# Kernel tuning notes

Hardware: AMD Instinct MI355X
Metric: run time of the kernel (lower is better)

The kernel has to match this reference:

```python
import jax, jax.numpy as jnp
import numpy as np

D = 512; NH = 8; NL = 6; DFF = 2048
TOK = 1024; APP = 3; V = TOK + APP; PAD = V - 1
B = 256; SENC = 16; LTGT = 62


def setup_inputs() -> dict:
    key = jax.random.key(0)
    ks = jax.random.split(key, 14)
    g = lambda k, shp, s=0.02: jax.random.normal(k, shp, jnp.float32) * s
    return dict(
        encoder_out=jax.random.normal(ks[0], (B, SENC, D), jnp.float32),
        point_out=jax.random.normal(ks[1], (B, D), jnp.float32),
        emb=g(ks[2], (V, D)),
        pos_embed=g(ks[3], (1, LTGT, D)),
        sa_inw=g(ks[4], (NL, 3 * D, D)), sa_inb=jnp.zeros((NL, 3 * D), jnp.float32),
        sa_outw=g(ks[5], (NL, D, D)), sa_outb=jnp.zeros((NL, D), jnp.float32),
        ca_inw=g(ks[6], (NL, 3 * D, D)), ca_inb=jnp.zeros((NL, 3 * D), jnp.float32),
        ca_outw=g(ks[7], (NL, D, D)), ca_outb=jnp.zeros((NL, D), jnp.float32),
        ln1_s=jnp.ones((NL, D), jnp.float32), ln1_b=jnp.zeros((NL, D), jnp.float32),
        ln2_s=jnp.ones((NL, D), jnp.float32), ln2_b=jnp.zeros((NL, D), jnp.float32),
        ln3_s=jnp.ones((NL, D), jnp.float32), ln3_b=jnp.zeros((NL, D), jnp.float32),
        ff1_w=g(ks[8], (NL, DFF, D)), ff1_b=jnp.zeros((NL, DFF), jnp.float32),
        ff2_w=g(ks[9], (NL, D, DFF)), ff2_b=jnp.zeros((NL, D), jnp.float32),
        out_w=g(ks[10], (V, D)), out_b=jnp.zeros((V,), jnp.float32),
        tgt=jax.random.randint(ks[11], (B, LTGT), 0, TOK),
    )


def _ln(x, s, b, eps=1e-5):
    m = x.mean(-1, keepdims=True)
    v = ((x - m) ** 2).mean(-1, keepdims=True)
    return (x - m) / jnp.sqrt(v + eps) * s + b


def _mha(q_in, kv_in, inw, inb, outw, outb, mask):
    # PyTorch MultiheadAttention with packed in_proj [3D, D]
    hd = D // NH
    wq, wk, wv = inw[:D], inw[D:2 * D], inw[2 * D:]
    bq, bk, bv = inb[:D], inb[D:2 * D], inb[2 * D:]
    Bq, Tq = q_in.shape[0], q_in.shape[1]
    Tk = kv_in.shape[1]
    q = (q_in @ wq.T + bq).reshape(Bq, Tq, NH, hd)
    k = (kv_in @ wk.T + bk).reshape(Bq, Tk, NH, hd)
    v = (kv_in @ wv.T + bv).reshape(Bq, Tk, NH, hd)
    s = jnp.einsum('bqhd,bkhd->bhqk', q, k) / np.float32(np.sqrt(hd))
    if mask is not None:
        s = s + mask
    a = jax.nn.softmax(s, axis=-1)
    o = jnp.einsum('bhqk,bkhd->bqhd', a, v).reshape(Bq, Tq, D)
    return o @ outw.T + outb


def reference(encoder_out, point_out, emb, pos_embed,
              sa_inw, sa_inb, sa_outw, sa_outb,
              ca_inw, ca_inb, ca_outw, ca_outb,
              ln1_s, ln1_b, ln2_s, ln2_b, ln3_s, ln3_b,
              ff1_w, ff1_b, ff2_w, ff2_b, out_w, out_b, tgt):
    # scheduled_sampling_ratio == 1.0 => the per-step loop always writes the
    # ground-truth token, so output_sequence == tgt[:, :-1] and the returned
    # tensor equals one full causal decoder pass over tgt[:, :-1].
    tokens = tgt[:, :-1]                      # [B, L], L = 61
    L = tokens.shape[1]
    neg = jnp.float32(-jnp.inf)
    causal = jnp.where(jnp.triu(jnp.ones((L, L), bool), 1), neg, 0.0)
    padm = jnp.where(tokens == PAD, neg, 0.0)[:, None, None, :]  # [B,1,1,L]
    mask = causal[None, None] + padm          # [B,1,L,L]
    mem = encoder_out[:, :1, :]               # memory length 1 (encoder_out[:, [0]])
    x = emb[tokens] + point_out[:, None, :] + pos_embed[0, :L]
    for i in range(NL):
        x = _ln(x + _mha(x, x, sa_inw[i], sa_inb[i], sa_outw[i], sa_outb[i], mask), ln1_s[i], ln1_b[i])
        x = _ln(x + _mha(x, mem, ca_inw[i], ca_inb[i], ca_outw[i], ca_outb[i], None), ln2_s[i], ln2_b[i])
        h = jax.nn.relu(x @ ff1_w[i].T + ff1_b[i]) @ ff2_w[i].T + ff2_b[i]
        x = _ln(x + h, ln3_s[i], ln3_b[i])
    return x @ out_w.T + out_b               # [B, L, V]
```

## Files before the change

kernel.cpp:

```cpp
#include <hip/hip_runtime.h>
#include <stdint.h>
#include <stddef.h>

typedef unsigned short u16;
typedef float f4 __attribute__((ext_vector_type(4)));
typedef float f32x4 __attribute__((ext_vector_type(4)));
typedef short bf16x8 __attribute__((ext_vector_type(8)));
typedef u16 u16x4 __attribute__((ext_vector_type(4)));
typedef int i4v __attribute__((ext_vector_type(4)));

#define PAD_TOK 1026
#define LQ 61
#define NBATCH 256
#define MTOT (NBATCH * LQ)

__device__ __forceinline__ u16 f2b(float f) {
  uint32_t x = __float_as_uint(f);
  x += 0x7fff + ((x >> 16) & 1);
  return (u16)(x >> 16);
}
__device__ __forceinline__ float b2f(u16 u) {
  return __uint_as_float(((uint32_t)u) << 16);
}

#define GLDS(gptr, lptr) __builtin_amdgcn_global_load_lds( \
    (const __attribute__((address_space(1))) void*)(gptr), \
    (__attribute__((address_space(3))) void*)(lptr), 16, 0, 0)

__device__ __forceinline__ bf16x8 ldfrag(const u16* buf, int row, int ksl, int kg) {
  const int chunk = (ksl * 4 + kg) ^ (row & 7);
  return *(const bf16x8*)&buf[row * 64 + chunk * 8];
}

template<int BM>
__global__ __launch_bounds__(256) void gemm_bt(
    const u16* __restrict__ A, const u16* __restrict__ W,
    const float* __restrict__ bias,
    float* __restrict__ Cf, u16* __restrict__ Cb,
    int M, int N, int K, int Nreal, int ldc, int relu,
    long aZ, long wZ, long bZ, long cZ)
{
  constexpr int MI = BM / 32;
  const int z = blockIdx.z;
  A += z * aZ; W += z * wZ; bias += z * bZ;
  if (Cf) Cf += z * cZ;
  if (Cb) Cb += z * cZ;

  __shared__ u16 As[BM * 64];
  __shared__ u16 Bs[128 * 64];

  const int gx = gridDim.x;
  const int nwg = gx * gridDim.y;
  const int orig = blockIdx.y * gx + blockIdx.x;
  const int q8 = nwg >> 3, r8 = nwg & 7;
  const int xcd = orig & 7, off = orig >> 3;
  const int nid = (xcd < r8 ? xcd * (q8 + 1) : r8 * (q8 + 1) + (xcd - r8) * q8) + off;
  const int bx = nid % gx, by = nid / gx;

  const int tid = threadIdx.x;
  const int wid = tid >> 6, lane = tid & 63;
  const int wr = wid >> 1, wc = wid & 1;
  const long m0 = (long)by * BM;
  const long n0 = (long)bx * 128;

  const int lr = lane >> 3;
  const int lc = lane & 7;
  const int scol = ((lc ^ lr) << 3);

  f32x4 acc[MI][4];
#pragma unroll
  for (int i = 0; i < MI; ++i)
#pragma unroll
    for (int j = 0; j < 4; ++j) acc[i][j] = (f32x4){0.f, 0.f, 0.f, 0.f};

  const u16* Abase = A + m0 * K;
  const u16* Wbase = W + n0 * K;
  const int r = lane & 15, kg = lane >> 4;

  for (int kt = 0; kt < K; kt += 64) {
#pragma unroll
    for (int c = 0; c < BM / 32; ++c) {
      const int row = wid * (BM / 4) + c * 8;
      GLDS(Abase + (long)(row + lr) * K + kt + scol, &As[row * 64]);
    }
#pragma unroll
    for (int c = 0; c < 4; ++c) {
      const int row = wid * 32 + c * 8;
      GLDS(Wbase + (long)(row + lr) * K + kt + scol, &Bs[row * 64]);
    }
    __syncthreads();

#pragma unroll
    for (int ks = 0; ks < 2; ++ks) {
      bf16x8 a[MI], b[4];
#pragma unroll
      for (int mi = 0; mi < MI; ++mi)
        a[mi] = ldfrag(As, wr * (BM / 2) + mi * 16 + r, ks, kg);
#pragma unroll
      for (int ni = 0; ni < 4; ++ni)
        b[ni] = ldfrag(Bs, wc * 64 + ni * 16 + r, ks, kg);
#pragma unroll
      for (int mi = 0; mi < MI; ++mi)
#pragma unroll
        for (int ni = 0; ni < 4; ++ni)
          acc[mi][ni] = __builtin_amdgcn_mfma_f32_16x16x32_bf16(a[mi], b[ni], acc[mi][ni], 0, 0, 0);
    }
    __syncthreads();
  }

  const int cr4 = (lane >> 4) * 4;
  const int cc = lane & 15;

  if (Cb) {
#pragma unroll
    for (int ni = 0; ni < 4; ++ni) {
      const int coll = wc * 64 + ni * 16 + cc;
      const float bv = bias[(int)n0 + coll];
#pragma unroll
      for (int mi = 0; mi < MI; ++mi) {
#pragma unroll
        for (int j = 0; j < 4; ++j) {
          const int rowl = wr * (BM / 2) + mi * 16 + cr4 + j;
          float v = acc[mi][ni][j] + bv;
          if (relu) v = fmaxf(v, 0.f);
          const int sw = (rowl & 7) << 3;
          u16* half = (coll & 64) ? Bs : As;
          half[rowl * 64 + ((coll & 63) ^ sw)] = f2b(v);
        }
      }
    }
    __syncthreads();
    constexpr int PT = BM / 16;
#pragma unroll
    for (int i = 0; i < PT; ++i) {
      const int t = i * 256 + tid;
      const int row = t >> 4, ch = t & 15;
      const int n = (int)n0 + ch * 8;
      if (n < Nreal) {
        const int phys = (ch & 7) ^ (row & 7);
        const u16* half = (ch < 8) ? As : Bs;
        bf16x8 vv = *(const bf16x8*)&half[row * 64 + phys * 8];
        *(bf16x8*)&Cb[(m0 + row) * (long)N + n] = vv;
      }
    }
  } else {
#pragma unroll
    for (int ni = 0; ni < 4; ++ni) {
      const int n = (int)n0 + wc * 64 + ni * 16 + cc;
      if (n >= Nreal) continue;
      const float bv = bias[n];
#pragma unroll
      for (int mi = 0; mi < MI; ++mi) {
#pragma unroll
        for (int j = 0; j < 4; ++j) {
          const long m = m0 + wr * (BM / 2) + mi * 16 + cr4 + j;
          float v = acc[mi][ni][j] + bv;
          if (relu) v = fmaxf(v, 0.f);
          Cf[m * ldc + n] = v;
        }
      }
    }
  }
}

template<bool CA2>
__global__ __launch_bounds__(512) void gemmln_k(
    const u16* __restrict__ A, const u16* __restrict__ W,
    const float* __restrict__ bias,
    const u16* __restrict__ cavb,
    const float* __restrict__ s1w, const float* __restrict__ b1w,
    const float* __restrict__ s2w, const float* __restrict__ b2w,
    u16* __restrict__ XB, int K)
{
  __shared__ u16 LDSBUF[2][36864];
  __shared__ float LSTAT[64][8];
  __shared__ u16 LCAV[1536];
  u16* const EP = &LDSBUF[0][0];

  const int nwg = gridDim.x;
  const int orig = blockIdx.x;
  const int q8 = nwg >> 3, r8 = nwg & 7;
  const int xcd = orig & 7, off = orig >> 3;
  const int by = (xcd < r8 ? xcd * (q8 + 1) : r8 * (q8 + 1) + (xcd - r8) * q8) + off;

  const int tid = threadIdx.x;
  const int wid = tid >> 6, lane = tid & 63;
  const int wm = wid >> 2, wn = wid & 3;
  const long m0 = (long)by * 64;

  const int lr = lane >> 3, lc = lane & 7;
  const int scol = ((lc ^ lr) << 3);
  const int r = lane & 15, kg = lane >> 4;

  f32x4 acc[2][8];
#pragma unroll
  for (int i = 0; i < 2; ++i)
#pragma unroll
    for (int j = 0; j < 8; ++j) acc[i][j] = (f32x4){0.f, 0.f, 0.f, 0.f};

  const u16* Abase = A + m0 * K;

#define STAGE(buf, kt) do {                                              \
    const int arow_ = wid * 8;                                           \
    GLDS(Abase + (long)(arow_ + lr) * K + (kt) + scol,                   \
         &(buf)[32768 + arow_ * 64]);                                    \
    _Pragma("unroll")                                                    \
    for (int c_ = 0; c_ < 8; ++c_) {                                     \
      const int row_ = wid * 64 + c_ * 8;                                \
      GLDS(W + (long)(row_ + lr) * K + (kt) + scol, &(buf)[row_ * 64]);  \
    }                                                                    \
  } while (0)

  const int nt = K >> 6;
  STAGE(LDSBUF[0], 0);
  asm volatile("s_waitcnt vmcnt(0)" ::: "memory");
  __builtin_amdgcn_sched_barrier(0);
  __builtin_amdgcn_s_barrier();

  for (int t = 0; t < nt; ++t) {
    u16* const bufc = &LDSBUF[t & 1][0];
    if (t + 1 < nt) STAGE(LDSBUF[(t + 1) & 1], (t + 1) << 6);
#pragma unroll
    for (int ks = 0; ks < 2; ++ks) {
      bf16x8 a0 = ldfrag(bufc + 32768, wm * 32 + r, ks, kg);
      bf16x8 a1 = ldfrag(bufc + 32768, wm * 32 + 16 + r, ks, kg);
      __builtin_amdgcn_s_setprio(1);
#pragma unroll
      for (int ni = 0; ni < 8; ++ni) {
        bf16x8 b = ldfrag(bufc, wn * 128 + ni * 16 + r, ks, kg);
        acc[0][ni] = __builtin_amdgcn_mfma_f32_16x16x32_bf16(a0, b, acc[0][ni], 0, 0, 0);
        acc[1][ni] = __builtin_amdgcn_mfma_f32_16x16x32_bf16(a1, b, acc[1][ni], 0, 0, 0);
      }
      __builtin_amdgcn_s_setprio(0);
    }
    asm volatile("s_waitcnt vmcnt(0)" ::: "memory");
    __builtin_amdgcn_sched_barrier(0);
    __builtin_amdgcn_s_barrier();
  }
#undef STAGE

  const int b0 = (int)(m0 / LQ);
  const int bsplit1 = (b0 + 1) * LQ;
  const int bsplit2 = (b0 + 2) * LQ;

#pragma unroll
  for (int i = 0; i < 8; ++i) {
    const int t = i * 512 + tid;
    const int row = t >> 6, ch = t & 63;
    *(bf16x8*)&EP[row * 516 + ch * 8] =
        *(const bf16x8*)&XB[(m0 + row) * 512 + ch * 8];
  }
  if constexpr (CA2) {
    for (int t = tid; t < 1536; t += 512) {
      const int bb = t >> 9, c = t & 511;
      int bi = b0 + bb;
      if (bi > NBATCH - 1) bi = NBATCH - 1;
      LCAV[bb * 512 + c] = cavb[(long)bi * 512 + c];
    }
  }
  __syncthreads();

  float bcol[8];
#pragma unroll
  for (int ni = 0; ni < 8; ++ni) bcol[ni] = bias[wn * 128 + ni * 16 + r];
#pragma unroll
  for (int mi = 0; mi < 2; ++mi)
#pragma unroll
    for (int ni = 0; ni < 8; ++ni) {
      const int col = wn * 128 + ni * 16 + r;
#pragma unroll
      for (int j = 0; j < 4; ++j) {
        const int row = wm * 32 + mi * 16 + kg * 4 + j;
        acc[mi][ni][j] += bcol[ni] + b2f(EP[row * 516 + col]);
      }
    }

#pragma unroll
  for (int mi = 0; mi < 2; ++mi)
#pragma unroll
    for (int j = 0; j < 4; ++j) {
      float s1 = 0.f, s2 = 0.f;
#pragma unroll
      for (int ni = 0; ni < 8; ++ni) {
        const float v = acc[mi][ni][j];
        s1 += v; s2 += v * v;
      }
#pragma unroll
      for (int o = 1; o < 16; o <<= 1) {
        s1 += __shfl_xor(s1, o);
        s2 += __shfl_xor(s2, o);
      }
      if (r == 0) {
        const int row = wm * 32 + mi * 16 + kg * 4 + j;
        LSTAT[row][wn] = s1;
        LSTAT[row][4 + wn] = s2;
      }
    }
  __syncthreads();

  float sc[8], bc[8];
#pragma unroll
  for (int ni = 0; ni < 8; ++ni) {
    const int col = wn * 128 + ni * 16 + r;
    sc[ni] = s1w[col]; bc[ni] = b1w[col];
  }
#pragma unroll
  for (int mi = 0; mi < 2; ++mi)
#pragma unroll
    for (int j = 0; j < 4; ++j) {
      const int row = wm * 32 + mi * 16 + kg * 4 + j;
      const float S1 = LSTAT[row][0] + LSTAT[row][1] + LSTAT[row][2] + LSTAT[row][3];
      const float S2 = LSTAT[row][4] + LSTAT[row][5] + LSTAT[row][6] + LSTAT[row][7];
      const float mean = S1 * (1.f / 512.f);
      const float var = S2 * (1.f / 512.f) - mean * mean;
      const float rstd = rsqrtf(var + 1e-5f);
#pragma unroll
      for (int ni = 0; ni < 8; ++ni)
        acc[mi][ni][j] = (acc[mi][ni][j] - mean) * rstd * sc[ni] + bc[ni];
    }

  if constexpr (CA2) {
#pragma unroll
    for (int mi = 0; mi < 2; ++mi)
#pragma unroll
      for (int j = 0; j < 4; ++j) {
        const int row = wm * 32 + mi * 16 + kg * 4 + j;
        const int gr = (int)m0 + row;
        const int sel = (gr >= bsplit2) ? 2 : ((gr >= bsplit1) ? 1 : 0);
#pragma unroll
        for (int ni = 0; ni < 8; ++ni) {
          const int col = wn * 128 + ni * 16 + r;
          acc[mi][ni][j] += b2f(LCAV[sel * 512 + col]);
        }
      }
    __syncthreads();
#pragma unroll
    for (int mi = 0; mi < 2; ++mi)
#pragma unroll
      for (int j = 0; j < 4; ++j) {
        float s1 = 0.f, s2 = 0.f;
#pragma unroll
        for (int ni = 0; ni < 8; ++ni) {
          const float v = acc[mi][ni][j];
          s1 += v; s2 += v * v;
        }
#pragma unroll
        for (int o = 1; o < 16; o <<= 1) {
          s1 += __shfl_xor(s1, o);
          s2 += __shfl_xor(s2, o);
        }
        if (r == 0) {
          const int row = wm * 32 + mi * 16 + kg * 4 + j;
          LSTAT[row][wn] = s1;
          LSTAT[row][4 + wn] = s2;
        }
      }
    __syncthreads();
#pragma unroll
    for (int ni = 0; ni < 8; ++ni) {
      const int col = wn * 128 + ni * 16 + r;
      sc[ni] = s2w[col]; bc[ni] = b2w[col];
    }
#pragma unroll
    for (int mi = 0; mi < 2; ++mi)
#pragma unroll
      for (int j = 0; j < 4; ++j) {
        const int row = wm * 32 + mi * 16 + kg * 4 + j;
        const float S1 = LSTAT[row][0] + LSTAT[row][1] + LSTAT[row][2] + LSTAT[row][3];
        const float S2 = LSTAT[row][4] + LSTAT[row][5] + LSTAT[row][6] + LSTAT[row][7];
        const float mean = S1 * (1.f / 512.f);
        const float var = S2 * (1.f / 512.f) - mean * mean;
        const float rstd = rsqrtf(var + 1e-5f);
#pragma unroll
        for (int ni = 0; ni < 8; ++ni)
          acc[mi][ni][j] = (acc[mi][ni][j] - mean) * rstd * sc[ni] + bc[ni];
      }
  }

#pragma unroll
  for (int mi = 0; mi < 2; ++mi)
#pragma unroll
    for (int ni = 0; ni < 8; ++ni) {
      const int col = wn * 128 + ni * 16 + r;
#pragma unroll
      for (int j = 0; j < 4; ++j) {
        const int row = wm * 32 + mi * 16 + kg * 4 + j;
        EP[row * 516 + col] = f2b(acc[mi][ni][j]);
      }
    }
  __syncthreads();
#pragma unroll
  for (int i = 0; i < 8; ++i) {
    const int t = i * 512 + tid;
    const int row = t >> 6, ch = t & 63;
    *(bf16x8*)&XB[(m0 + row) * 512 + ch * 8] =
        *(const bf16x8*)&EP[row * 516 + ch * 8];
  }
}

__global__ __launch_bounds__(256) void attn_k(const u16* __restrict__ qkv,
                                              const int* __restrict__ tgt,
                                              u16* __restrict__ outp)
{
  __shared__ u16 Qs[64 * 72];
  __shared__ u16 Ks[64 * 72];
  __shared__ u16 Vt[64 * 72];
  __shared__ float S[64 * 65];
  __shared__ int stok[64];

  const int bid = blockIdx.x;
  const int b = bid >> 3, h = bid & 7;
  const int tid = threadIdx.x;
  const int tr = tid >> 2, seg = tid & 3;

  if (tid < 64) stok[tid] = (tid < 61) ? tgt[b * 62 + tid] : -1;

  const long rowbase = ((long)(b * LQ + tr)) * 1536 + h * 64;
  if (tr < LQ) {
    const i4v* qsrc = (const i4v*)(qkv + rowbase + seg * 16);
    i4v q0 = qsrc[0], q1 = qsrc[1];
    *(i4v*)&Qs[tr * 72 + seg * 16] = q0;
    *(i4v*)&Qs[tr * 72 + seg * 16 + 8] = q1;
    const i4v* ksrc = (const i4v*)(qkv + rowbase + 512 + seg * 16);
    i4v k0 = ksrc[0], k1 = ksrc[1];
    *(i4v*)&Ks[tr * 72 + seg * 16] = k0;
    *(i4v*)&Ks[tr * 72 + seg * 16 + 8] = k1;
    const u16* vsrc = qkv + rowbase + 1024 + seg * 16;
#pragma unroll
    for (int i = 0; i < 16; ++i) Vt[(seg * 16 + i) * 72 + tr] = vsrc[i];
  } else {
    i4v zz = {0, 0, 0, 0};
    *(i4v*)&Qs[tr * 72 + seg * 16] = zz;
    *(i4v*)&Qs[tr * 72 + seg * 16 + 8] = zz;
    *(i4v*)&Ks[tr * 72 + seg * 16] = zz;
    *(i4v*)&Ks[tr * 72 + seg * 16 + 8] = zz;
#pragma unroll
    for (int i = 0; i < 16; ++i) Vt[(seg * 16 + i) * 72 + tr] = 0;
  }
  __syncthreads();

  const int lane = tid & 63, w = tid >> 6;
  const int r = lane & 15, kg = lane >> 4;

  {
    f32x4 s[4];
#pragma unroll
    for (int ni = 0; ni < 4; ++ni) s[ni] = (f32x4){0.f, 0.f, 0.f, 0.f};
    bf16x8 a0 = *(const bf16x8*)&Qs[(w * 16 + r) * 72 + kg * 8];
    bf16x8 a1 = *(const bf16x8*)&Qs[(w * 16 + r) * 72 + 32 + kg * 8];
#pragma unroll
    for (int ni = 0; ni < 4; ++ni) {
      bf16x8 b0 = *(const bf16x8*)&Ks[(ni * 16 + r) * 72 + kg * 8];
      bf16x8 b1 = *(const bf16x8*)&Ks[(ni * 16 + r) * 72 + 32 + kg * 8];
      s[ni] = __builtin_amdgcn_mfma_f32_16x16x32_bf16(a0, b0, s[ni], 0, 0, 0);
      s[ni] = __builtin_amdgcn_mfma_f32_16x16x32_bf16(a1, b1, s[ni], 0, 0, 0);
    }
#pragma unroll
    for (int ni = 0; ni < 4; ++ni)
#pragma unroll
      for (int j = 0; j < 4; ++j)
        S[(w * 16 + kg * 4 + j) * 65 + ni * 16 + r] = s[ni][j];
  }
  __syncthreads();

  {
    const int row = tid >> 2, g = tid & 3;
    float vals[16];
    float mx = -3e38f;
#pragma unroll
    for (int i = 0; i < 16; ++i) {
      const int k = g * 16 + i;
      float v = S[row * 65 + k] * 0.125f;
      const bool ok = (k <= row) && (k < LQ) && (stok[k] != PAD_TOK);
      v = ok ? v : -1e30f;
      vals[i] = v;
      mx = fmaxf(mx, v);
    }
    mx = fmaxf(mx, __shfl_xor(mx, 1));
    mx = fmaxf(mx, __shfl_xor(mx, 2));
    float sum = 0.f;
#pragma unroll
    for (int i = 0; i < 16; ++i) { float e = __expf(vals[i] - mx); vals[i] = e; sum += e; }
    sum += __shfl_xor(sum, 1);
    sum += __shfl_xor(sum, 2);
    const float inv = 1.f / sum;
#pragma unroll
    for (int i = 0; i < 16; ++i) Qs[row * 72 + g * 16 + i] = f2b(vals[i] * inv);
  }
  __syncthreads();

  {
    f32x4 o[4];
#pragma unroll
    for (int ni = 0; ni < 4; ++ni) o[ni] = (f32x4){0.f, 0.f, 0.f, 0.f};
    bf16x8 a0 = *(const bf16x8*)&Qs[(w * 16 + r) * 72 + kg * 8];
    bf16x8 a1 = *(const bf16x8*)&Qs[(w * 16 + r) * 72 + 32 + kg * 8];
#pragma unroll
    for (int ni = 0; ni < 4; ++ni) {
      bf16x8 b0 = *(const bf16x8*)&Vt[(ni * 16 + r) * 72 + kg * 8];
      bf16x8 b1 = *(const bf16x8*)&Vt[(ni * 16 + r) * 72 + 32 + kg * 8];
      o[ni] = __builtin_amdgcn_mfma_f32_16x16x32_bf16(a0, b0, o[ni], 0, 0, 0);
      o[ni] = __builtin_amdgcn_mfma_f32_16x16x32_bf16(a1, b1, o[ni], 0, 0, 0);
    }
#pragma unroll
    for (int ni = 0; ni < 4; ++ni)
#pragma unroll
      for (int j = 0; j < 4; ++j) {
        const int qrow = w * 16 + kg * 4 + j;
        const int col = ni * 16 + r;
        Ks[qrow * 64 + (col ^ ((qrow & 7) << 3))] = f2b(o[ni][j]);
      }
  }
  __syncthreads();

  {
    const int row = tid >> 2, sub = tid & 3;
    if (row < LQ) {
      const long obase = ((long)(b * LQ + row)) * 512 + h * 64;
#pragma unroll
      for (int i = 0; i < 2; ++i) {
        const int ch = i * 4 + sub;
        const int phys = ch ^ (row & 7);
        bf16x8 vv = *(const bf16x8*)&Ks[row * 64 + phys * 8];
        *(bf16x8*)&outp[obase + ch * 8] = vv;
      }
    }
  }
}

__global__ __launch_bounds__(256) void embed_k(const float* __restrict__ emb,
                                               const float* __restrict__ pout,
                                               const float* __restrict__ pos,
                                               const int* __restrict__ tgt,
                                               u16* __restrict__ XB)
{
  const int m = blockIdx.x * 4 + (threadIdx.x >> 6);
  const int lane = threadIdx.x & 63;
  const int b = m / LQ, t = m % LQ;
  const int tok = tgt[b * 62 + t];
  const int d0 = lane * 8;
  const f4* e = (const f4*)(emb + (long)tok * 512 + d0);
  const f4* p = (const f4*)(pout + (long)b * 512 + d0);
  const f4* q = (const f4*)(pos + (long)t * 512 + d0);
  f4 v0 = e[0] + p[0] + q[0];
  f4 v1 = e[1] + p[1] + q[1];
  u16x4* xb = (u16x4*)(XB + (long)m * 512 + d0);
  xb[0] = (u16x4){f2b(v0[0]), f2b(v0[1]), f2b(v0[2]), f2b(v0[3])};
  xb[1] = (u16x4){f2b(v1[0]), f2b(v1[1]), f2b(v1[2]), f2b(v1[3])};
}

__global__ void cvtall_k(const float* __restrict__ s0, const float* __restrict__ s1,
                         const float* __restrict__ s2, const float* __restrict__ s3,
                         const float* __restrict__ s4,
                         u16* __restrict__ d0, u16* __restrict__ d1,
                         u16* __restrict__ d2, u16* __restrict__ d3,
                         u16* __restrict__ d4)
{
  const int N0 = 1179648;
  const int N1 = N0 + 393216;
  const int N2 = N1 + 393216;
  const int N3 = N2 + 1572864;
  const int N4 = N3 + 1572864;
  for (int i = blockIdx.x * 256 + threadIdx.x; i < N4; i += gridDim.x * 256) {
    const float* s; u16* d; int k;
    if (i < N0)      { s = s0; d = d0; k = i; }
    else if (i < N1) { s = s1; d = d1; k = i - N0; }
    else if (i < N2) { s = s2; d = d2; k = i - N1; }
    else if (i < N3) { s = s3; d = d3; k = i - N2; }
    else             { s = s4; d = d4; k = i - N3; }
    f4 v = ((const f4*)s)[k];
    ((u16x4*)d)[k] = (u16x4){f2b(v[0]), f2b(v[1]), f2b(v[2]), f2b(v[3])};
  }
}

__global__ void cvt_ca_v_k(const float* __restrict__ ca_inw, u16* __restrict__ dst) {
  const int i = blockIdx.x * 256 + threadIdx.x;
  if (i >= 393216) return;
  const int l = i >> 16, rem = i & 65535;
  f4 v = ((const f4*)ca_inw)[l * 196608 + 131072 + rem];
  ((u16x4*)dst)[i] = (u16x4){f2b(v[0]), f2b(v[1]), f2b(v[2]), f2b(v[3])};
}

__global__ void cvt_outw_k(const float* __restrict__ out_w, u16* __restrict__ dst) {
  const int i = blockIdx.x * 256 + threadIdx.x;
  if (i >= 147456) return;
  const int row = (i * 4) >> 9;
  u16x4 o = {0, 0, 0, 0};
  if (row < 1027) {
    f4 v = ((const f4*)out_w)[i];
    o = (u16x4){f2b(v[0]), f2b(v[1]), f2b(v[2]), f2b(v[3])};
  }
  ((u16x4*)dst)[i] = o;
}

__global__ void cvt_outb_k(const float* __restrict__ out_b, float* __restrict__ dst) {
  const int i = blockIdx.x * 256 + threadIdx.x;
  if (i >= 1152) return;
  dst[i] = (i < 1027) ? out_b[i] : 0.f;
}

__global__ void cvt_memb_k(const float* __restrict__ enc, u16* __restrict__ dst) {
  const int i = blockIdx.x * 256 + threadIdx.x;
  if (i >= 32768) return;
  const int b = (i * 4) >> 9, d = (i * 4) & 511;
  f4 v = ((const f4*)enc)[(b * 8192 + d) >> 2];
  ((u16x4*)dst)[i] = (u16x4){f2b(v[0]), f2b(v[1]), f2b(v[2]), f2b(v[3])};
}

static constexpr size_t XB_OFF    = 0;
static constexpr size_t BIG_OFF   = 15990784;
static constexpr size_t ATT_OFF   = 79953920;
static constexpr size_t WSA_OFF   = 95944704;
static constexpr size_t WSO_OFF   = 105381888;
static constexpr size_t WCAV_OFF  = 108527616;
static constexpr size_t WCO_OFF   = 111673344;
static constexpr size_t WF1_OFF   = 114819072;
static constexpr size_t WF2_OFF   = 127401984;
static constexpr size_t WOUT_OFF  = 139984896;
static constexpr size_t BOUT_OFF  = 141164544;
static constexpr size_t MEMB_OFF  = 141169152;
static constexpr size_t CATMP_OFF = 141431296;
static constexpr size_t CAVB_OFF  = 143004160;

extern "C" void kernel_launch(void* const* d_in, const int* in_sizes, int n_in,
                              void* d_out, int out_size, void* d_ws, size_t ws_size,
                              hipStream_t stream) {
  (void)in_sizes; (void)n_in; (void)out_size; (void)ws_size;
  const float* encoder_out = (const float*)d_in[0];
  const float* point_out   = (const float*)d_in[1];
  const float* emb         = (const float*)d_in[2];
  const float* pos         = (const float*)d_in[3];
  const float* sa_inw      = (const float*)d_in[4];
  const float* sa_inb      = (const float*)d_in[5];
  const float* sa_outw     = (const float*)d_in[6];
  const float* sa_outb     = (const float*)d_in[7];
  const float* ca_inw      = (const float*)d_in[8];
  const float* ca_inb      = (const float*)d_in[9];
  const float* ca_outw     = (const float*)d_in[10];
  const float* ca_outb     = (const float*)d_in[11];
  const float* ln1_s       = (const float*)d_in[12];
  const float* ln1_b       = (const float*)d_in[13];
  const float* ln2_s       = (const float*)d_in[14];
  const float* ln2_b       = (const float*)d_in[15];
  const float* ln3_s       = (const float*)d_in[16];
  const float* ln3_b       = (const float*)d_in[17];
  const float* ff1_w       = (const float*)d_in[18];
  const float* ff1_b       = (const float*)d_in[19];
  const float* ff2_w       = (const float*)d_in[20];
  const float* ff2_b       = (const float*)d_in[21];
  const float* out_w       = (const float*)d_in[22];
  const float* out_b       = (const float*)d_in[23];
  const int*   tgt         = (const int*)d_in[24];

  char* ws = (char*)d_ws;
  u16*   XB    = (u16*)(ws + XB_OFF);
  u16*   BIG   = (u16*)(ws + BIG_OFF);
  u16*   ATT   = (u16*)(ws + ATT_OFF);
  u16*   WSA   = (u16*)(ws + WSA_OFF);
  u16*   WSO   = (u16*)(ws + WSO_OFF);
  u16*   WCAV  = (u16*)(ws + WCAV_OFF);
  u16*   WCO   = (u16*)(ws + WCO_OFF);
  u16*   WF1   = (u16*)(ws + WF1_OFF);
  u16*   WF2   = (u16*)(ws + WF2_OFF);
  u16*   WOUT  = (u16*)(ws + WOUT_OFF);
  float* BOUT  = (float*)(ws + BOUT_OFF);
  u16*   MEMB  = (u16*)(ws + MEMB_OFF);
  u16*   CATMP = (u16*)(ws + CATMP_OFF);
  u16*   CAVB  = (u16*)(ws + CAVB_OFF);

  cvtall_k<<<dim3(2048), dim3(256), 0, stream>>>(
      sa_inw, sa_outw, ca_outw, ff1_w, ff2_w, WSA, WSO, WCO, WF1, WF2);
  cvt_ca_v_k<<<dim3(1536), dim3(256), 0, stream>>>(ca_inw, WCAV);
  cvt_outw_k<<<dim3(576), dim3(256), 0, stream>>>(out_w, WOUT);
  cvt_outb_k<<<dim3(5), dim3(256), 0, stream>>>(out_b, BOUT);
  cvt_memb_k<<<dim3(128), dim3(256), 0, stream>>>(encoder_out, MEMB);

  embed_k<<<dim3(MTOT / 4), dim3(256), 0, stream>>>(emb, point_out, pos, tgt, XB);

  gemm_bt<64><<<dim3(4, 4, 6), dim3(256), 0, stream>>>(
      MEMB, WCAV, ca_inb + 1024, nullptr, CATMP,
      256, 512, 512, 512, 512, 0,
      0L, 262144L, 1536L, 131072L);
  gemm_bt<64><<<dim3(4, 4, 6), dim3(256), 0, stream>>>(
      CATMP, WCO, ca_outb, nullptr, CAVB,
      256, 512, 512, 512, 512, 0,
      131072L, 262144L, 512L, 131072L);

  for (int l = 0; l < 6; ++l) {
    gemm_bt<128><<<dim3(12, 122, 1), dim3(256), 0, stream>>>(
        XB, WSA + (long)l * 786432, sa_inb + l * 1536, nullptr, BIG,
        MTOT, 1536, 512, 1536, 1536, 0, 0L, 0L, 0L, 0L);
    attn_k<<<dim3(2048), dim3(256), 0, stream>>>(BIG, tgt, ATT);
    gemmln_k<true><<<dim3(244), dim3(512), 0, stream>>>(
        ATT, WSO + (long)l * 262144, sa_outb + l * 512,
        CAVB + (long)l * 131072,
        ln1_s + l * 512, ln1_b + l * 512, ln2_s + l * 512, ln2_b + l * 512,
        XB, 512);
    gemm_bt<128><<<dim3(16, 122, 1), dim3(256), 0, stream>>>(
        XB, WF1 + (long)l * 1048576, ff1_b + l * 2048, nullptr, BIG,
        MTOT, 2048, 512, 2048, 2048, 1, 0L, 0L, 0L, 0L);
    gemmln_k<false><<<dim3(244), dim3(512), 0, stream>>>(
        BIG, WF2 + (long)l * 1048576, ff2_b + l * 512,
        nullptr,
        ln3_s + l * 512, ln3_b + l * 512, nullptr, nullptr,
        XB, 2048);
  }

  gemm_bt<128><<<dim3(9, 122, 1), dim3(256), 0, stream>>>(
      XB, WOUT, BOUT, (float*)d_out, nullptr,
      MTOT, 1152, 512, 1027, 1027, 0, 0L, 0L, 0L, 0L);
}
```

Measured before the change: 1.291 ms.

## Add 128x256 GEMM kernel and split FF2 GEMM from its layernorm

Result: faster. 1.124 ms (-13.0%).

```diff
diff --git a/kernel.cpp b/kernel.cpp
--- a/kernel.cpp
+++ b/kernel.cpp
@@ -30,6 +30,133 @@
 __device__ __forceinline__ bf16x8 ldfrag(const u16* buf, int row, int ksl, int kg) {
   const int chunk = (ksl * 4 + kg) ^ (row & 7);
   return *(const bf16x8*)&buf[row * 64 + chunk * 8];
+}
+
+__global__ __launch_bounds__(512) void gemm_bt2(
+    const u16* __restrict__ A, const u16* __restrict__ W,
+    const float* __restrict__ bias,
+    float* __restrict__ Cf, u16* __restrict__ Cb,
+    int N, int K, int Nreal, int ldc, int relu)
+{
+  __shared__ u16 SH[384 * 64];
+  u16* const As = SH;
+  u16* const Bs = SH + 8192;
+
+  const int gx = gridDim.x;
+  const int nwg = gx * gridDim.y;
+  const int orig = blockIdx.y * gx + blockIdx.x;
+  const int q8 = nwg >> 3, r8 = nwg & 7;
+  const int xcd = orig & 7, off = orig >> 3;
+  const int nid = (xcd < r8 ? xcd * (q8 + 1) : r8 * (q8 + 1) + (xcd - r8) * q8) + off;
+  const int bx = nid % gx, by = nid / gx;
+
+  const int tid = threadIdx.x;
+  const int wid = tid >> 6, lane = tid & 63;
+  const int wm = wid >> 2, wn = wid & 3;
+  const long m0 = (long)by * 128;
+  const long n0 = (long)bx * 256;
+
+  const int lr = lane >> 3;
+  const int lc = lane & 7;
+  const int scol = ((lc ^ lr) << 3);
+
+  f32x4 acc[4][4];
+#pragma unroll
+  for (int i = 0; i < 4; ++i)
+#pragma unroll
+    for (int j = 0; j < 4; ++j) acc[i][j] = (f32x4){0.f, 0.f, 0.f, 0.f};
+
+  const u16* Abase = A + m0 * K;
+  const u16* Wbase = W + n0 * K;
+  const int r = lane & 15, kg = lane >> 4;
+
+  for (int kt = 0; kt < K; kt += 64) {
+#pragma unroll
+    for (int c = 0; c < 2; ++c) {
+      const int row = wid * 16 + c * 8;
+      GLDS(Abase + (long)(row + lr) * K + kt + scol, &As[row * 64]);
+    }
+#pragma unroll
+    for (int c = 0; c < 4; ++c) {
+      const int row = wid * 32 + c * 8;
+      GLDS(Wbase + (long)(row + lr) * K + kt + scol, &Bs[row * 64]);
+    }
+    __syncthreads();
+
+#pragma unroll
+    for (int ks = 0; ks < 2; ++ks) {
+      bf16x8 a[4], b[4];
+#pragma unroll
+      for (int mi = 0; mi < 4; ++mi)
+        a[mi] = ldfrag(As, wm * 64 + mi * 16 + r, ks, kg);
+#pragma unroll
+      for (int ni = 0; ni < 4; ++ni)
+        b[ni] = ldfrag(Bs, wn * 64 + ni * 16 + r, ks, kg);
+#pragma unroll
+      for (int mi = 0; mi < 4; ++mi)
+#pragma unroll
+        for (int ni = 0; ni < 4; ++ni)
+          acc[mi][ni] = __builtin_amdgcn_mfma_f32_16x16x32_bf16(a[mi], b[ni], acc[mi][ni], 0, 0, 0);
+    }
+    __syncthreads();
+  }
+
+  const int cr4 = (lane >> 4) * 4;
+  const int cc = lane & 15;
+
+  if (Cb) {
+#pragma unroll
+    for (int half = 0; half < 2; ++half) {
+      if (wm == half) {
+#pragma unroll
+        for (int ni = 0; ni < 4; ++ni) {
+          const int coll = wn * 64 + ni * 16 + cc;
+          const float bv = bias[(int)n0 + coll];
+#pragma unroll
+          for (int mi = 0; mi < 4; ++mi) {
+#pragma unroll
+            for (int j = 0; j < 4; ++j) {
+              const int rowl = mi * 16 + cr4 + j;
+              float v = acc[mi][ni][j] + bv;
+              if (relu) v = fmaxf(v, 0.f);
+              const int phys = (coll >> 3) ^ (rowl & 31);
+              SH[rowl * 256 + phys * 8 + (coll & 7)] = f2b(v);
+            }
+          }
+        }
+      }
+      __syncthreads();
+#pragma unroll
+      for (int i = 0; i < 4; ++i) {
+        const int t = i * 512 + tid;
+        const int row = t >> 5, ch = t & 31;
+        const int n = (int)n0 + ch * 8;
+        if (n < Nreal) {
+          const int phys = ch ^ (row & 31);
+          *(bf16x8*)&Cb[(m0 + half * 64 + row) * (long)N + n] =
+              *(const bf16x8*)&SH[row * 256 + phys * 8];
+        }
+      }
+      __syncthreads();
+    }
+  } else {
+#pragma unroll
+    for (int ni = 0; ni < 4; ++ni) {
+      const int n = (int)n0 + wn * 64 + ni * 16 + cc;
+      if (n >= Nreal) continue;
+      const float bv = bias[n];
+#pragma unroll
+      for (int mi = 0; mi < 4; ++mi) {
+#pragma unroll
+        for (int j = 0; j < 4; ++j) {
+          const long m = m0 + wm * 64 + mi * 16 + cr4 + j;
+          float v = acc[mi][ni][j] + bv;
+          if (relu) v = fmaxf(v, 0.f);
+          Cf[m * ldc + n] = v;
+        }
+      }
+    }
+  }
 }
 
 template<int BM>
@@ -163,7 +290,6 @@
   }
 }
 
-template<bool CA2>
 __global__ __launch_bounds__(512) void gemmln_k(
     const u16* __restrict__ A, const u16* __restrict__ W,
     const float* __restrict__ bias,
@@ -250,13 +376,11 @@
     *(bf16x8*)&EP[row * 516 + ch * 8] =
         *(const bf16x8*)&XB[(m0 + row) * 512 + ch * 8];
   }
-  if constexpr (CA2) {
-    for (int t = tid; t < 1536; t += 512) {
-      const int bb = t >> 9, c = t & 511;
-      int bi = b0 + bb;
-      if (bi > NBATCH - 1) bi = NBATCH - 1;
-      LCAV[bb * 512 + c] = cavb[(long)bi * 512 + c];
-    }
+  for (int t = tid; t < 1536; t += 512) {
+    const int bb = t >> 9, c = t & 511;
+    int bi = b0 + bb;
+    if (bi > NBATCH - 1) bi = NBATCH - 1;
+    LCAV[bb * 512 + c] = cavb[(long)bi * 512 + c];
   }
   __syncthreads();
 
@@ -319,63 +443,61 @@
         acc[mi][ni][j] = (acc[mi][ni][j] - mean) * rstd * sc[ni] + bc[ni];
     }
 
-  if constexpr (CA2) {
-#pragma unroll
-    for (int mi = 0; mi < 2; ++mi)
-#pragma unroll
-      for (int j = 0; j < 4; ++j) {
+#pragma unroll
+  for (int mi = 0; mi < 2; ++mi)
+#pragma unroll
+    for (int j = 0; j < 4; ++j) {
+      const int row = wm * 32 + mi * 16 + kg * 4 + j;
+      const int gr = (int)m0 + row;
+      const int sel = (gr >= bsplit2) ? 2 : ((gr >= bsplit1) ? 1 : 0);
+#pragma unroll
+      for (int ni = 0; ni < 8; ++ni) {
+        const int col = wn * 128 + ni * 16 + r;
+        acc[mi][ni][j] += b2f(LCAV[sel * 512 + col]);
+      }
+    }
+  __syncthreads();
+#pragma unroll
+  for (int mi = 0; mi < 2; ++mi)
+#pragma unroll
+    for (int j = 0; j < 4; ++j) {
+      float s1 = 0.f, s2 = 0.f;
+#pragma unroll
+      for (int ni = 0; ni < 8; ++ni) {
+        const float v = acc[mi][ni][j];
+        s1 += v; s2 += v * v;
+      }
+#pragma unroll
+      for (int o = 1; o < 16; o <<= 1) {
+        s1 += __shfl_xor(s1, o);
+        s2 += __shfl_xor(s2, o);
+      }
+      if (r == 0) {
         const int row = wm * 32 + mi * 16 + kg * 4 + j;
-        const int gr = (int)m0 + row;
-        const int sel = (gr >= bsplit2) ? 2 : ((gr >= bsplit1) ? 1 : 0);
-#pragma unroll
-        for (int ni = 0; ni < 8; ++ni) {
-          const int col = wn * 128 + ni * 16 + r;
-          acc[mi][ni][j] += b2f(LCAV[sel * 512 + col]);
-        }
-      }
-    __syncthreads();
-#pragma unroll
-    for (int mi = 0; mi < 2; ++mi)
-#pragma unroll
-      for (int j = 0; j < 4; ++j) {
-        float s1 = 0.f, s2 = 0.f;
-#pragma unroll
-        for (int ni = 0; ni < 8; ++ni) {
-          const float v = acc[mi][ni][j];
-          s1 += v; s2 += v * v;
-        }
-#pragma unroll
-        for (int o = 1; o < 16; o <<= 1) {
-          s1 += __shfl_xor(s1, o);
-          s2 += __shfl_xor(s2, o);
-        }
-        if (r == 0) {
-          const int row = wm * 32 + mi * 16 + kg * 4 + j;
-          LSTAT[row][wn] = s1;
-          LSTAT[row][4 + wn] = s2;
-        }
-      }
-    __syncthreads();
-#pragma unroll
-    for (int ni = 0; ni < 8; ++ni) {
-      const int col = wn * 128 + ni * 16 + r;
-      sc[ni] = s2w[col]; bc[ni] = b2w[col];
-    }
-#pragma unroll
-    for (int mi = 0; mi < 2; ++mi)
-#pragma unroll
-      for (int j = 0; j < 4; ++j) {
-        const int row = wm * 32 + mi * 16 + kg * 4 + j;
-        const float S1 = LSTAT[row][0] + LSTAT[row][1] + LSTAT[row][2] + LSTAT[row][3];
-        const float S2 = LSTAT[row][4] + LSTAT[row][5] + LSTAT[row][6] + LSTAT[row][7];
-        const float mean = S1 * (1.f / 512.f);
-        const float var = S2 * (1.f / 512.f) - mean * mean;
-        const float rstd = rsqrtf(var + 1e-5f);
-#pragma unroll
-        for (int ni = 0; ni < 8; ++ni)
-          acc[mi][ni][j] = (acc[mi][ni][j] - mean) * rstd * sc[ni] + bc[ni];
-      }
-  }
+        LSTAT[row][wn] = s1;
+        LSTAT[row][4 + wn] = s2;
+      }
+    }
+  __syncthreads();
+#pragma unroll
+  for (int ni = 0; ni < 8; ++ni) {
+    const int col = wn * 128 + ni * 16 + r;
+    sc[ni] = s2w[col]; bc[ni] = b2w[col];
+  }
+#pragma unroll
+  for (int mi = 0; mi < 2; ++mi)
+#pragma unroll
+    for (int j = 0; j < 4; ++j) {
+      const int row = wm * 32 + mi * 16 + kg * 4 + j;
+      const float S1 = LSTAT[row][0] + LSTAT[row][1] + LSTAT[row][2] + LSTAT[row][3];
+      const float S2 = LSTAT[row][4] + LSTAT[row][5] + LSTAT[row][6] + LSTAT[row][7];
+      const float mean = S1 * (1.f / 512.f);
+      const float var = S2 * (1.f / 512.f) - mean * mean;
+      const float rstd = rsqrtf(var + 1e-5f);
+#pragma unroll
+      for (int ni = 0; ni < 8; ++ni)
+        acc[mi][ni][j] = (acc[mi][ni][j] - mean) * rstd * sc[ni] + bc[ni];
+    }
 
 #pragma unroll
   for (int mi = 0; mi < 2; ++mi)
@@ -526,6 +648,53 @@
       }
     }
   }
+}
+
+__device__ __forceinline__ void ln_row(f4& v0, f4& v1,
+                                       const float* __restrict__ sw,
+                                       const float* __restrict__ bw, int d0) {
+  float s1 = v0[0] + v0[1] + v0[2] + v0[3] + v1[0] + v1[1] + v1[2] + v1[3];
+  float s2 = v0[0]*v0[0] + v0[1]*v0[1] + v0[2]*v0[2] + v0[3]*v0[3]
+           + v1[0]*v1[0] + v1[1]*v1[1] + v1[2]*v1[2] + v1[3]*v1[3];
+#pragma unroll
+  for (int off = 1; off < 64; off <<= 1) {
+    s1 += __shfl_xor(s1, off);
+    s2 += __shfl_xor(s2, off);
+  }
+  const float mean = s1 * (1.f / 512.f);
+  const float var = s2 * (1.f / 512.f) - mean * mean;
+  const float rstd = rsqrtf(var + 1e-5f);
+  const f4* sp = (const f4*)(sw + d0);
+  const f4* bp = (const f4*)(bw + d0);
+  f4 ss0 = sp[0], ss1 = sp[1], bb0 = bp[0], bb1 = bp[1];
+#pragma unroll
+  for (int i = 0; i < 4; ++i) {
+    v0[i] = (v0[i] - mean) * rstd * ss0[i] + bb0[i];
+    v1[i] = (v1[i] - mean) * rstd * ss1[i] + bb1[i];
+  }
+}
+
+__global__ __launch_bounds__(256) void lnf3_k(const u16* __restrict__ p,
+                                              const u16* __restrict__ xr,
+                                              const float* __restrict__ s1,
+                                              const float* __restrict__ b1,
+                                              u16* __restrict__ out)
+{
+  const int m = blockIdx.x * 4 + (threadIdx.x >> 6);
+  const int lane = threadIdx.x & 63;
+  const int d0 = lane * 8;
+  bf16x8 pv = *(const bf16x8*)(p + (long)m * 512 + d0);
+  bf16x8 xv = *(const bf16x8*)(xr + (long)m * 512 + d0);
+  f4 v0, v1;
+#pragma unroll
+  for (int i = 0; i < 4; ++i) {
+    v0[i] = b2f((u16)pv[i]) + b2f((u16)xv[i]);
+    v1[i] = b2f((u16)pv[4 + i]) + b2f((u16)xv[4 + i]);
+  }
+  ln_row(v0, v1, s1, b1, d0);
+  u16x4* ob = (u16x4*)(out + (long)m * 512 + d0);
+  ob[0] = (u16x4){f2b(v0[0]), f2b(v0[1]), f2b(v0[2]), f2b(v0[3])};
+  ob[1] = (u16x4){f2b(v1[0]), f2b(v1[1]), f2b(v1[2]), f2b(v1[3])};
 }
 
 __global__ __launch_bounds__(256) void embed_k(const float* __restrict__ emb,
@@ -583,7 +752,7 @@
 
 __global__ void cvt_outw_k(const float* __restrict__ out_w, u16* __restrict__ dst) {
   const int i = blockIdx.x * 256 + threadIdx.x;
-  if (i >= 147456) return;
+  if (i >= 163840) return;
   const int row = (i * 4) >> 9;
   u16x4 o = {0, 0, 0, 0};
   if (row < 1027) {
@@ -595,7 +764,7 @@
 
 __global__ void cvt_outb_k(const float* __restrict__ out_b, float* __restrict__ dst) {
   const int i = blockIdx.x * 256 + threadIdx.x;
-  if (i >= 1152) return;
+  if (i >= 1280) return;
   dst[i] = (i < 1027) ? out_b[i] : 0.f;
 }
 
@@ -608,19 +777,20 @@
 }
 
 static constexpr size_t XB_OFF    = 0;
-static constexpr size_t BIG_OFF   = 15990784;
-static constexpr size_t ATT_OFF   = 79953920;
-static constexpr size_t WSA_OFF   = 95944704;
-static constexpr size_t WSO_OFF   = 105381888;
-static constexpr size_t WCAV_OFF  = 108527616;
-static constexpr size_t WCO_OFF   = 111673344;
-static constexpr size_t WF1_OFF   = 114819072;
-static constexpr size_t WF2_OFF   = 127401984;
-static constexpr size_t WOUT_OFF  = 139984896;
-static constexpr size_t BOUT_OFF  = 141164544;
-static constexpr size_t MEMB_OFF  = 141169152;
-static constexpr size_t CATMP_OFF = 141431296;
-static constexpr size_t CAVB_OFF  = 143004160;
+static constexpr size_t P_OFF     = 15990784;
+static constexpr size_t BIG_OFF   = 31981568;
+static constexpr size_t ATT_OFF   = 95944704;
+static constexpr size_t WSA_OFF   = 111935488;
+static constexpr size_t WSO_OFF   = 121372672;
+static constexpr size_t WCAV_OFF  = 124518400;
+static constexpr size_t WCO_OFF   = 127664128;
+static constexpr size_t WF1_OFF   = 130809856;
+static constexpr size_t WF2_OFF   = 143392768;
+static constexpr size_t WOUT_OFF  = 155975680;
+static constexpr size_t BOUT_OFF  = 157286400;
+static constexpr size_t MEMB_OFF  = 157291520;
+static constexpr size_t CATMP_OFF = 157553664;
+static constexpr size_t CAVB_OFF  = 159126528;
 
 extern "C" void kernel_launch(void* const* d_in, const int* in_sizes, int n_in,
                               void* d_out, int out_size, void* d_ws, size_t ws_size,
@@ -654,6 +824,7 @@
 
   char* ws = (char*)d_ws;
   u16*   XB    = (u16*)(ws + XB_OFF);
+  u16*   P     = (u16*)(ws + P_OFF);
   u16*   BIG   = (u16*)(ws + BIG_OFF);
   u16*   ATT   = (u16*)(ws + ATT_OFF);
   u16*   WSA   = (u16*)(ws + WSA_OFF);
@@ -671,7 +842,7 @@
   cvtall_k<<<dim3(2048), dim3(256), 0, stream>>>(
       sa_inw, sa_outw, ca_outw, ff1_w, ff2_w, WSA, WSO, WCO, WF1, WF2);
   cvt_ca_v_k<<<dim3(1536), dim3(256), 0, stream>>>(ca_inw, WCAV);
-  cvt_outw_k<<<dim3(576), dim3(256), 0, stream>>>(out_w, WOUT);
+  cvt_outw_k<<<dim3(640), dim3(256), 0, stream>>>(out_w, WOUT);
   cvt_outb_k<<<dim3(5), dim3(256), 0, stream>>>(out_b, BOUT);
   cvt_memb_k<<<dim3(128), dim3(256), 0, stream>>>(encoder_out, MEMB);
 
@@ -687,26 +858,26 @@
       131072L, 262144L, 512L, 131072L);
 
   for (int l = 0; l < 6; ++l) {
-    gemm_bt<128><<<dim3(12, 122, 1), dim3(256), 0, stream>>>(
+    gemm_bt2<<<dim3(6, 122), dim3(512), 0, stream>>>(
         XB, WSA + (long)l * 786432, sa_inb + l * 1536, nullptr, BIG,
-        MTOT, 1536, 512, 1536, 1536, 0, 0L, 0L, 0L, 0L);
+        1536, 512, 1536, 1536, 0);
     attn_k<<<dim3(2048), dim3(256), 0, stream>>>(BIG, tgt, ATT);
-    gemmln_k<true><<<dim3(244), dim3(512), 0, stream>>>(
+    gemmln_k<<<dim3(244), dim3(512), 0, stream>>>(
         ATT, WSO + (long)l * 262144, sa_outb + l * 512,
         CAVB + (long)l * 131072,
         ln1_s + l * 512, ln1_b + l * 512, ln2_s + l * 512, ln2_b + l * 512,
         XB, 512);
-    gemm_bt<128><<<dim3(16, 122, 1), dim3(256), 0, stream>>>(
+    gemm_bt2<<<dim3(8, 122), dim3(512), 0, stream>>>(
         XB, WF1 + (long)l * 1048576, ff1_b + l * 2048, nullptr, BIG,
-        MTOT, 2048, 512, 2048, 2048, 1, 0L, 0L, 0L, 0L);
-    gemmln_k<false><<<dim3(244), dim3(512), 0, stream>>>(
-        BIG, WF2 + (long)l * 1048576, ff2_b + l * 512,
-        nullptr,
-        ln3_s + l * 512, ln3_b + l * 512, nullptr, nullptr,
-        XB, 2048);
-  }
-
-  gemm_bt<128><<<dim3(9, 122, 1), dim3(256), 0, stream>>>(
+        2048, 512, 2048, 2048, 1);
+    gemm_bt<64><<<dim3(4, 244, 1), dim3(256), 0, stream>>>(
+        BIG, WF2 + (long)l * 1048576, ff2_b + l * 512, nullptr, P,
+        MTOT, 512, 2048, 512, 512, 0, 0L, 0L, 0L, 0L);
+    lnf3_k<<<dim3(MTOT / 4), dim3(256), 0, stream>>>(
+        P, XB, ln3_s + l * 512, ln3_b + l * 512, XB);
+  }
+
+  gemm_bt2<<<dim3(5, 122), dim3(512), 0, stream>>>(
       XB, WOUT, BOUT, (float*)d_out, nullptr,
-      MTOT, 1152, 512, 1027, 1027, 0, 0L, 0L, 0L, 0L);
-}
+      1280, 512, 1027, 1027, 0);
+}
```
